# Kernel optimization log

Measured on AMD Instinct MI355X. Metric: run time of the kernel, lower is better.

The kernel has to match this reference:

```python
import jax, jax.numpy as jnp
import numpy as np

B, L, H = 512, 50, 128
HEADS, K = 8, 3
LP = 2.0            # l_p for LPPool1d
NUM_NODE = 250000


def setup_inputs() -> dict:
    key = jax.random.key(0)
    ks = jax.random.split(key, 24)
    s = 0.09  # ~1/sqrt(hidden) init as in reset_parameters
    p = lambda k, shp: jax.random.normal(k, shp, jnp.float32) * s
    return {
        "hidden": jax.random.normal(ks[0], (B, L, H), jnp.float32),
        "mask": jnp.ones((B, L), jnp.int32),
        "emb_w": p(ks[1], (NUM_NODE, H)),
        "pos_w": p(ks[2], (200, H)),
        "w1": p(ks[3], (2 * H, H)),
        "w2": p(ks[4], (H, 1)),
        "glu1_w": p(ks[5], (H, H)), "glu1_b": p(ks[6], (H,)),
        "glu2_w": p(ks[7], (H, H)),
        "lq_w0": p(ks[8], (H, H)), "lq_b0": p(ks[9], (H,)),
        "lq_w1": p(ks[10], (2 * H, H)), "lq_b1": p(ks[11], (H,)),
        "lq_w2": p(ks[12], (3 * H, H)), "lq_b2": p(ks[13], (H,)),
        "wz": p(ks[14], (H, H)), "bz": p(ks[15], (H,)),
        "wo": p(ks[16], (H, H)), "bo": p(ks[17], (H,)),
        "wt": p(ks[18], (H, H)), "bt": p(ks[19], (H,)),
        "lt2_w": p(ks[20], (2 * H, H)), "lt2_b": p(ks[21], (H,)),
    }


def reference(hidden, mask, emb_w, pos_w, w1, w2, glu1_w, glu1_b, glu2_w,
              lq_w0, lq_b0, lq_w1, lq_b1, lq_w2, lq_b2,
              wz, bz, wo, bo, wt, bt, lt2_w, lt2_b):
    Bc, Lc, Hc = hidden.shape
    dh = Hc // HEADS
    maskf = mask.astype(hidden.dtype)[:, :, None]          # [B,L,1]
    lengths = jnp.sum(mask, axis=1)                         # [B]

    # soft-attention readout (w_1 / w_2 / glu1 / glu2)
    pos = jnp.broadcast_to(pos_w[:Lc][None], (Bc, Lc, Hc))
    hs = jnp.sum(hidden * maskf, axis=1) / jnp.sum(maskf, axis=1)   # [B,H]
    nh = jnp.tanh(jnp.concatenate([pos, hidden], -1) @ w1)
    nh = jax.nn.sigmoid(nh @ glu1_w + glu1_b + (hs @ glu2_w)[:, None, :])
    beta = (nh @ w2) * maskf                                # [B,L,1]
    select = jnp.sum(beta * hidden, axis=1)                 # [B,H]

    # last-k item gathers feeding linear_q
    bidx = jnp.arange(Bc)
    def last_vec(j):
        idx = jnp.clip(lengths - (j + 1), -1, 1000)
        idx = jnp.where(idx < 0, idx + Lc, idx)  # torch negative-index wrap
        return hidden[bidx, idx]
    lasts = [last_vec(j) for j in range(K)]
    lq = [(lq_w0, lq_b0), (lq_w1, lq_b1), (lq_w2, lq_b2)]
    hts = jnp.stack([jnp.concatenate(lasts[:i + 1], -1) @ lq[i][0] + lq[i][1]
                     for i in range(K)], axis=1)            # [B,K,H]
    hts = hts / (jnp.linalg.norm(hts, axis=1, keepdims=True) + 1e-12)
    ht0 = hidden[bidx, lengths - 1]                         # [B,H]

    # LastAttenion (eval mode: dropout off); reshapes replicate torch .view
    q0 = (hts @ wz + bz).reshape(-1, K, dh)                 # [B*heads,K,dh]
    q1 = (hidden @ wo + bo).reshape(-1, Lc, dh)             # [B*heads,L,dh]
    q2 = (hidden @ wt + bt).reshape(-1, Lc, dh)
    alpha = jax.nn.sigmoid(jnp.einsum('bkd,bld->bkl', q0, q1))
    alpha = alpha.reshape(Bc, K * HEADS, Lc).transpose(0, 2, 1)  # [B,L,K*heads]
    alpha = jax.nn.softmax(2 * alpha, axis=1)
    # LPPool1d(norm=LP, kernel=K, stride=K) over last dim -> [B,L,heads]
    pooled = jnp.sum(alpha.reshape(Bc, Lc, HEADS, K) ** LP, axis=-1) ** (1.0 / LP)
    alpha = jnp.where(mask[:, :, None] > 0, pooled, -jnp.inf)
    alpha = jax.nn.softmax(2 * alpha, axis=1)               # [B,L,heads]
    q2r = q2.reshape(Bc, Lc, HEADS, dh)
    ais = jnp.sum((alpha[..., None] * q2r).reshape(Bc, Lc, Hc) * maskf, axis=1)  # [B,H]

    a = jnp.concatenate([ais, ht0], 1) @ lt2_w + lt2_b
    session = (select + a) * 0.5
    session = session / (jnp.linalg.norm(session, axis=1, keepdims=True) + 1e-12)
    b_items = emb_w[1:]
    b_items = b_items / (jnp.linalg.norm(b_items, axis=1, keepdims=True) + 1e-12)
    return 16.0 * (session @ b_items.T)                     # [B, num_node-1]
```

## Files before the change

### kernel.cpp

```cpp
#include <hip/hip_runtime.h>

#define LB 50
#define NITEMS 249999

__device__ __forceinline__ float sigm(float x){ return 1.0f/(1.0f + __expf(-x)); }

__device__ __forceinline__ unsigned int pack2(float x, float y){
  unsigned int a = __float_as_uint(x), b = __float_as_uint(y);
  a = (a + 0x7fffu + ((a>>16)&1u)) >> 16;
  b = (b + 0x7fffu + ((b>>16)&1u)) >> 16;
  return a | (b<<16);
}

__global__ void k_pos_part(const float* __restrict__ pos_w, const float* __restrict__ w1,
                           float* __restrict__ pos_part){
  int l = blockIdx.x, h = threadIdx.x;
  __shared__ float pr[128];
  pr[h] = pos_w[l*128 + h];
  __syncthreads();
  float s = 0.f;
  for (int j = 0; j < 128; ++j) s += pr[j] * w1[j*128 + h];
  pos_part[l*128 + h] = s;
}

__global__ void k_batch_prep(const float* __restrict__ hidden, const int* __restrict__ mask,
                             float* __restrict__ hs, float* __restrict__ lastsc,
                             float* __restrict__ ht0v){
  int b = blockIdx.x, h = threadIdx.x;
  const float* hb = hidden + (size_t)b*LB*128;
  const int* mb = mask + b*LB;
  int len = 0; float msum = 0.f, acc = 0.f;
  for (int l = 0; l < LB; ++l){
    int mi = mb[l];
    float mf = (float)mi;
    len += mi;
    msum += mf;
    acc += hb[l*128 + h] * mf;
  }
  hs[b*128+h] = acc / msum;
  for (int j = 0; j < 3; ++j){
    int idx = len - 1 - j;
    if (idx < -1) idx = -1;
    if (idx < 0) idx += LB;
    lastsc[b*384 + j*128 + h] = hb[idx*128 + h];
  }
  int i0 = len - 1; if (i0 < 0) i0 += LB;
  ht0v[b*128+h] = hb[i0*128 + h];
}

template<int MODE>
__global__ __launch_bounds__(256) void k_gemmA(const float* __restrict__ IN,
      const float* __restrict__ W, const float* __restrict__ extra,
      const float* __restrict__ w2, const int* __restrict__ mask,
      float* __restrict__ OUT){
  __shared__ float hidL[64*129];
  __shared__ float red[64*17];
  int t = threadIdx.x;
  int r0 = blockIdx.x * 64;
  for (int i = 0; i < 32; ++i){
    int p = i*256 + t;
    int row = p >> 7, k = p & 127;
    hidL[row*129 + k] = IN[(size_t)(r0+row)*128 + k];
  }
  __syncthreads();
  int tx = t & 15, ty = t >> 4;
  float acc[4][8];
#pragma unroll
  for (int m=0;m<4;++m)
#pragma unroll
    for (int c=0;c<8;++c) acc[m][c]=0.f;
  for (int k = 0; k < 128; ++k){
    float4 wa = *(const float4*)&W[k*128 + tx*4];
    float4 wb = *(const float4*)&W[k*128 + 64 + tx*4];
#pragma unroll
    for (int m = 0; m < 4; ++m){
      float a = hidL[(ty*4+m)*129 + k];
      acc[m][0] += a*wa.x; acc[m][1] += a*wa.y; acc[m][2] += a*wa.z; acc[m][3] += a*wa.w;
      acc[m][4] += a*wb.x; acc[m][5] += a*wb.y; acc[m][6] += a*wb.z; acc[m][7] += a*wb.w;
    }
  }
  if constexpr (MODE == 0){
#pragma unroll
    for (int m=0;m<4;++m){
      int r = r0 + ty*4 + m; int l = r % 50;
#pragma unroll
      for (int ci=0;ci<4;++ci){
        int c = tx*4+ci;
        OUT[(size_t)r*128 + c] = tanhf(acc[m][ci] + extra[l*128+c]);
        c = 64 + tx*4 + ci;
        OUT[(size_t)r*128 + c] = tanhf(acc[m][4+ci] + extra[l*128+c]);
      }
    }
  } else if constexpr (MODE == 1){
#pragma unroll
    for (int m=0;m<4;++m){
      int r = r0 + ty*4 + m; int bb = r / 50;
      float part = 0.f;
#pragma unroll
      for (int ci=0;ci<4;++ci){
        int c = tx*4+ci;
        float s = sigm(acc[m][ci] + extra[bb*128+c]); part += s * w2[c];
        c = 64 + tx*4 + ci;
        s = sigm(acc[m][4+ci] + extra[bb*128+c]); part += s * w2[c];
      }
      red[(ty*4+m)*17 + tx] = part;
    }
    __syncthreads();
    if (t < 64){
      float s = 0.f;
      for (int x=0;x<16;++x) s += red[t*17+x];
      int r = r0 + t;
      OUT[r] = s * (float)mask[r];
    }
  } else {
#pragma unroll
    for (int m=0;m<4;++m){
      int r = r0 + ty*4 + m;
#pragma unroll
      for (int ci=0;ci<4;++ci){
        int c = tx*4+ci;
        OUT[(size_t)r*128 + c] = acc[m][ci] + extra[c];
        c = 64 + tx*4 + ci;
        OUT[(size_t)r*128 + c] = acc[m][4+ci] + extra[c];
      }
    }
  }
}

__global__ void k_hsg(const float* __restrict__ hs, const float* __restrict__ glu2_w,
                      const float* __restrict__ glu1_b, float* __restrict__ hsg){
  int b = blockIdx.x, h = threadIdx.x;
  __shared__ float hl[128];
  hl[h] = hs[b*128+h];
  __syncthreads();
  float s = glu1_b[h];
  for (int j=0;j<128;++j) s += hl[j]*glu2_w[j*128+h];
  hsg[b*128+h] = s;
}

__global__ void k_select(const float* __restrict__ beta, const float* __restrict__ hidden,
                         float* __restrict__ sel){
  int b = blockIdx.x, h = threadIdx.x;
  float s = 0.f;
  for (int l=0;l<LB;++l) s += beta[b*LB+l]*hidden[((size_t)b*LB+l)*128 + h];
  sel[b*128+h] = s;
}

__global__ void k_hts_q0(const float* __restrict__ lastsc,
   const float* __restrict__ lq_w0, const float* __restrict__ lq_b0,
   const float* __restrict__ lq_w1, const float* __restrict__ lq_b1,
   const float* __restrict__ lq_w2, const float* __restrict__ lq_b2,
   const float* __restrict__ wz, const float* __restrict__ bz,
   float* __restrict__ q0f){
  int b = blockIdx.x, h = threadIdx.x;
  __shared__ float ll[384];
  __shared__ float htsL[384];
  for (int i=h;i<384;i+=128) ll[i]=lastsc[b*384+i];
  __syncthreads();
  float h0 = lq_b0[h], h1 = lq_b1[h], h2 = lq_b2[h];
  for (int j=0;j<128;++j) h0 += ll[j]*lq_w0[j*128+h];
  for (int j=0;j<256;++j) h1 += ll[j]*lq_w1[j*128+h];
  for (int j=0;j<384;++j) h2 += ll[j]*lq_w2[j*128+h];
  float nrm = sqrtf(h0*h0+h1*h1+h2*h2) + 1e-12f;
  htsL[h] = h0/nrm; htsL[128+h] = h1/nrm; htsL[256+h] = h2/nrm;
  __syncthreads();
  for (int k=0;k<3;++k){
    float s = bz[h];
    for (int j=0;j<128;++j) s += htsL[k*128+j]*wz[j*128+h];
    q0f[b*384 + k*128 + h] = s;
  }
}

__global__ __launch_bounds__(256) void k_attn(const float* __restrict__ q0f,
    const float* __restrict__ q1f, const float* __restrict__ q2f,
    const int* __restrict__ mask, float* __restrict__ ais){
  int b = blockIdx.x, t = threadIdx.x;
  __shared__ float q0L[384];
  __shared__ float q1L[6400];
  __shared__ float S[1200];
  __shared__ float A_[400];
  __shared__ float mkL[50];
  for (int i=t;i<384;i+=256) q0L[i]=q0f[b*384+i];
  for (int i=t;i<6400;i+=256) q1L[i]=q1f[(size_t)b*6400+i];
  if (t<50) mkL[t] = (float)mask[b*50+t];
  __syncthreads();
  for (int idx=t; idx<1200; idx+=256){
    int c = idx/50, l = idx - c*50;
    int g = c/3, kk = c - g*3;
    const float* q0p = q0L + 48*g + 16*kk;
    const float* q1p = q1L + 800*g + 16*l;
    float d = 0.f;
#pragma unroll
    for (int dd=0;dd<16;++dd) d += q0p[dd]*q1p[dd];
    S[c*50+l] = 2.f*sigm(d);
  }
  __syncthreads();
  if (t < 24){
    float m = -1e30f;
    for (int l=0;l<50;++l) m = fmaxf(m, S[t*50+l]);
    float s = 0.f;
    for (int l=0;l<50;++l){ float e=__expf(S[t*50+l]-m); S[t*50+l]=e; s+=e; }
    float inv = 1.f/s;
    for (int l=0;l<50;++l) S[t*50+l] *= inv;
  }
  __syncthreads();
  if (t < 8){
    int g = t;
    float m = -1e30f;
    for (int l=0;l<50;++l){
      float a0=S[(3*g+0)*50+l], a1=S[(3*g+1)*50+l], a2=S[(3*g+2)*50+l];
      float p = sqrtf(a0*a0+a1*a1+a2*a2);
      float v = (mkL[l] > 0.f) ? 2.f*p : -1e30f;
      A_[l*8+g]=v; m=fmaxf(m,v);
    }
    float s=0.f;
    for (int l=0;l<50;++l){ float e=__expf(A_[l*8+g]-m); A_[l*8+g]=e; s+=e; }
    float inv=1.f/s;
    for (int l=0;l<50;++l) A_[l*8+g]*=inv;
  }
  __syncthreads();
  if (t < 128){
    int h=t; float acc=0.f;
    for (int l=0;l<50;++l) acc += A_[l*8+(h>>4)] * q2f[((size_t)b*50+l)*128+h] * mkL[l];
    ais[b*128+h]=acc;
  }
}

__global__ void k_session(const float* __restrict__ ais, const float* __restrict__ ht0v,
   const float* __restrict__ sel, const float* __restrict__ lt2_w, const float* __restrict__ lt2_b,
   float* __restrict__ session){
  int b = blockIdx.x, h = threadIdx.x;
  __shared__ float aL[128];
  __shared__ float hL[128];
  __shared__ float red[128];
  aL[h]=ais[b*128+h]; hL[h]=ht0v[b*128+h];
  __syncthreads();
  float a = lt2_b[h];
  for (int j=0;j<128;++j) a += aL[j]*lt2_w[j*128+h];
  for (int j=0;j<128;++j) a += hL[j]*lt2_w[(128+j)*128+h];
  float s = (sel[b*128+h] + a)*0.5f;
  red[h]=s*s; __syncthreads();
  for (int off=64; off>0; off>>=1){
    if (h<off) red[h]+=red[h+off];
    __syncthreads();
  }
  session[b*128+h] = s / (sqrtf(red[0]) + 1e-12f);
}

__global__ __launch_bounds__(256) void k_invnorm(const float* __restrict__ emb, float* __restrict__ invn){
  int t = threadIdx.x;
  int row = blockIdx.x*4 + (t>>6);
  int lane = t & 63;
  if (row >= NITEMS) return;
  float2 v = *(const float2*)&emb[(size_t)(1+row)*128 + lane*2];
  float ss = v.x*v.x + v.y*v.y;
  for (int off=32; off; off>>=1) ss += __shfl_down(ss, off, 64);
  if (lane==0) invn[row] = 16.f/(sqrtf(ss)+1e-12f);
}

typedef short bhalf8 __attribute__((ext_vector_type(8)));
typedef float f32x4 __attribute__((ext_vector_type(4)));

__global__ __launch_bounds__(256) void k_out(const float* __restrict__ session,
    const float* __restrict__ emb, const float* __restrict__ invn, float* __restrict__ out){
  __shared__ unsigned int Ab[128*64];
  __shared__ unsigned int Bbuf[128*64];
  int t = threadIdx.x;
  int mb = blockIdx.x & 3, nb = blockIdx.x >> 2;
  int m0 = mb*128, n0 = nb*128;
  for (int i=0;i<32;++i){
    int p = i*256 + t;
    int row = p >> 6, kp = p & 63;
    float2 v = *(const float2*)&session[(size_t)(m0+row)*128 + kp*2];
    Ab[row*64 + (((kp>>2) ^ (row&7))<<2) + (kp&3)] = pack2(v.x, v.y);
  }
  for (int i=0;i<32;++i){
    int p = i*256 + t;
    int row = p >> 6, kp = p & 63;
    int item = n0 + row;
    float2 v = {0.f, 0.f};
    float sc = 0.f;
    if (item < NITEMS){ v = *(const float2*)&emb[(size_t)(1+item)*128 + kp*2]; sc = invn[item]; }
    Bbuf[row*64 + (((kp>>2) ^ (row&7))<<2) + (kp&3)] = pack2(v.x*sc, v.y*sc);
  }
  __syncthreads();
  int lane = t & 63, w = t >> 6;
  int r16 = lane & 15, quad = lane >> 4;
  f32x4 acc[2][8];
#pragma unroll
  for (int mi=0;mi<2;++mi)
#pragma unroll
    for (int ni=0;ni<8;++ni) acc[mi][ni] = (f32x4){0.f,0.f,0.f,0.f};
#pragma unroll
  for (int kc=0;kc<4;++kc){
    int gq = kc*4 + quad;
    bhalf8 af[2], bf[8];
#pragma unroll
    for (int mi=0;mi<2;++mi){
      int row = w*32 + mi*16 + r16;
      af[mi] = *(const bhalf8*)&Ab[row*64 + ((gq ^ (row&7))<<2)];
    }
#pragma unroll
    for (int ni=0;ni<8;++ni){
      int row = ni*16 + r16;
      bf[ni] = *(const bhalf8*)&Bbuf[row*64 + ((gq ^ (row&7))<<2)];
    }
#pragma unroll
    for (int mi=0;mi<2;++mi)
#pragma unroll
      for (int ni=0;ni<8;++ni)
        acc[mi][ni] = __builtin_amdgcn_mfma_f32_16x16x32_bf16(af[mi], bf[ni], acc[mi][ni], 0,0,0);
  }
#pragma unroll
  for (int mi=0;mi<2;++mi){
    int gr0 = m0 + w*32 + mi*16 + quad*4;
#pragma unroll
    for (int ni=0;ni<8;++ni){
      int gc = n0 + ni*16 + r16;
      if (gc < NITEMS){
#pragma unroll
        for (int r=0;r<4;++r) out[(size_t)(gr0+r)*NITEMS + gc] = acc[mi][ni][r];
      }
    }
  }
}

extern "C" void kernel_launch(void* const* d_in, const int* in_sizes, int n_in,
                              void* d_out, int out_size, void* d_ws, size_t ws_size,
                              hipStream_t stream){
  const float* hidden = (const float*)d_in[0];
  const int*   mask   = (const int*)d_in[1];
  const float* emb_w  = (const float*)d_in[2];
  const float* pos_w  = (const float*)d_in[3];
  const float* w1     = (const float*)d_in[4];
  const float* w2     = (const float*)d_in[5];
  const float* glu1_w = (const float*)d_in[6];
  const float* glu1_b = (const float*)d_in[7];
  const float* glu2_w = (const float*)d_in[8];
  const float* lq_w0  = (const float*)d_in[9];
  const float* lq_b0  = (const float*)d_in[10];
  const float* lq_w1  = (const float*)d_in[11];
  const float* lq_b1  = (const float*)d_in[12];
  const float* lq_w2  = (const float*)d_in[13];
  const float* lq_b2  = (const float*)d_in[14];
  const float* wz     = (const float*)d_in[15];
  const float* bz     = (const float*)d_in[16];
  const float* wo     = (const float*)d_in[17];
  const float* bo     = (const float*)d_in[18];
  const float* wt     = (const float*)d_in[19];
  const float* bt     = (const float*)d_in[20];
  const float* lt2_w  = (const float*)d_in[21];
  const float* lt2_b  = (const float*)d_in[22];
  float* outp = (float*)d_out;

  float* ws = (float*)d_ws;
  size_t o = 0;
  float* pos_part = ws + o; o += 50*128;
  float* hs       = ws + o; o += 512*128;
  float* hsg      = ws + o; o += 512*128;
  float* lastsc   = ws + o; o += 512*384;
  float* ht0v     = ws + o; o += 512*128;
  float* beta     = ws + o; o += 25600;
  float* sel      = ws + o; o += 512*128;
  float* q0f      = ws + o; o += 512*384;
  float* ais      = ws + o; o += 512*128;
  float* session  = ws + o; o += 512*128;
  float* invn     = ws + o; o += 250000;
  float* big1     = ws + o; o += (size_t)25600*128;
  float* big2     = ws + o; o += (size_t)25600*128;

  k_pos_part<<<50,128,0,stream>>>(pos_w, w1, pos_part);
  k_batch_prep<<<512,128,0,stream>>>(hidden, mask, hs, lastsc, ht0v);
  k_gemmA<0><<<400,256,0,stream>>>(hidden, w1 + 128*128, pos_part, nullptr, nullptr, big1);
  k_hsg<<<512,128,0,stream>>>(hs, glu2_w, glu1_b, hsg);
  k_gemmA<1><<<400,256,0,stream>>>(big1, glu1_w, hsg, w2, mask, beta);
  k_select<<<512,128,0,stream>>>(beta, hidden, sel);
  k_hts_q0<<<512,128,0,stream>>>(lastsc, lq_w0,lq_b0,lq_w1,lq_b1,lq_w2,lq_b2, wz, bz, q0f);
  k_gemmA<2><<<400,256,0,stream>>>(hidden, wo, bo, nullptr, nullptr, big1);
  k_gemmA<2><<<400,256,0,stream>>>(hidden, wt, bt, nullptr, nullptr, big2);
  k_attn<<<512,256,0,stream>>>(q0f, big1, big2, mask, ais);
  k_session<<<512,128,0,stream>>>(ais, ht0v, sel, lt2_w, lt2_b, session);
  k_invnorm<<<62500,256,0,stream>>>(emb_w, invn);
  k_out<<<7816,256,0,stream>>>(session, emb_w, invn, outp);
}
```

Measured before the change: 1.182 ms.

## Restructure output GEMM to keep item tile in registers and loop over batch

The final scoring GEMM now assigns each block 128 items for all 512 session rows. The normalized bf16 item fragments are held in registers and reused across four batch chunks, instead of reloading and re-converting the embedding tile for every batch chunk. The session vectors are pre-converted to bf16 in k_session and read directly from global/L2 without LDS staging. MFMA operands are swapped so each lane holds four consecutive output columns, which allows float4 output stores. This removes LDS traffic and quadruple embedding reads, at the cost of uncoalesced row-strided session loads and more register pressure.

```diff
diff --git a/kernel.cpp b/kernel.cpp
--- a/kernel.cpp
+++ b/kernel.cpp
@@ -10,6 +10,12 @@
   a = (a + 0x7fffu + ((a>>16)&1u)) >> 16;
   b = (b + 0x7fffu + ((b>>16)&1u)) >> 16;
   return a | (b<<16);
+}
+
+__device__ __forceinline__ unsigned short bf16of(float x){
+  unsigned int a = __float_as_uint(x);
+  a = (a + 0x7fffu + ((a>>16)&1u)) >> 16;
+  return (unsigned short)a;
 }
 
 __global__ void k_pos_part(const float* __restrict__ pos_w, const float* __restrict__ w1,
@@ -228,7 +234,7 @@
 
 __global__ void k_session(const float* __restrict__ ais, const float* __restrict__ ht0v,
    const float* __restrict__ sel, const float* __restrict__ lt2_w, const float* __restrict__ lt2_b,
-   float* __restrict__ session){
+   float* __restrict__ session, unsigned short* __restrict__ sbf){
   int b = blockIdx.x, h = threadIdx.x;
   __shared__ float aL[128];
   __shared__ float hL[128];
@@ -244,7 +250,9 @@
     if (h<off) red[h]+=red[h+off];
     __syncthreads();
   }
-  session[b*128+h] = s / (sqrtf(red[0]) + 1e-12f);
+  float v = s / (sqrtf(red[0]) + 1e-12f);
+  session[b*128+h] = v;
+  sbf[b*128+h] = bf16of(v);
 }
 
 __global__ __launch_bounds__(256) void k_invnorm(const float* __restrict__ emb, float* __restrict__ invn){
@@ -261,65 +269,73 @@
 typedef short bhalf8 __attribute__((ext_vector_type(8)));
 typedef float f32x4 __attribute__((ext_vector_type(4)));
 
-__global__ __launch_bounds__(256) void k_out(const float* __restrict__ session,
+struct f4a { float x, y, z, w; };
+
+__global__ __launch_bounds__(256) void k_out(const unsigned short* __restrict__ sbf,
     const float* __restrict__ emb, const float* __restrict__ invn, float* __restrict__ out){
-  __shared__ unsigned int Ab[128*64];
-  __shared__ unsigned int Bbuf[128*64];
   int t = threadIdx.x;
-  int mb = blockIdx.x & 3, nb = blockIdx.x >> 2;
-  int m0 = mb*128, n0 = nb*128;
-  for (int i=0;i<32;++i){
-    int p = i*256 + t;
-    int row = p >> 6, kp = p & 63;
-    float2 v = *(const float2*)&session[(size_t)(m0+row)*128 + kp*2];
-    Ab[row*64 + (((kp>>2) ^ (row&7))<<2) + (kp&3)] = pack2(v.x, v.y);
-  }
-  for (int i=0;i<32;++i){
-    int p = i*256 + t;
-    int row = p >> 6, kp = p & 63;
-    int item = n0 + row;
-    float2 v = {0.f, 0.f};
-    float sc = 0.f;
-    if (item < NITEMS){ v = *(const float2*)&emb[(size_t)(1+item)*128 + kp*2]; sc = invn[item]; }
-    Bbuf[row*64 + (((kp>>2) ^ (row&7))<<2) + (kp&3)] = pack2(v.x*sc, v.y*sc);
-  }
-  __syncthreads();
+  int n0 = blockIdx.x * 128;
   int lane = t & 63, w = t >> 6;
   int r16 = lane & 15, quad = lane >> 4;
-  f32x4 acc[2][8];
-#pragma unroll
-  for (int mi=0;mi<2;++mi)
-#pragma unroll
-    for (int ni=0;ni<8;++ni) acc[mi][ni] = (f32x4){0.f,0.f,0.f,0.f};
-#pragma unroll
-  for (int kc=0;kc<4;++kc){
-    int gq = kc*4 + quad;
-    bhalf8 af[2], bf[8];
-#pragma unroll
-    for (int mi=0;mi<2;++mi){
-      int row = w*32 + mi*16 + r16;
-      af[mi] = *(const bhalf8*)&Ab[row*64 + ((gq ^ (row&7))<<2)];
-    }
-#pragma unroll
-    for (int ni=0;ni<8;++ni){
-      int row = ni*16 + r16;
-      bf[ni] = *(const bhalf8*)&Bbuf[row*64 + ((gq ^ (row&7))<<2)];
-    }
-#pragma unroll
-    for (int mi=0;mi<2;++mi)
-#pragma unroll
-      for (int ni=0;ni<8;++ni)
-        acc[mi][ni] = __builtin_amdgcn_mfma_f32_16x16x32_bf16(af[mi], bf[ni], acc[mi][ni], 0,0,0);
-  }
-#pragma unroll
-  for (int mi=0;mi<2;++mi){
-    int gr0 = m0 + w*32 + mi*16 + quad*4;
-#pragma unroll
-    for (int ni=0;ni<8;++ni){
-      int gc = n0 + ni*16 + r16;
-      if (gc < NITEMS){
-#pragma unroll
-        for (int r=0;r<4;++r) out[(size_t)(gr0+r)*NITEMS + gc] = acc[mi][ni][r];
+
+  bhalf8 ef[2][4];
+#pragma unroll
+  for (int ni2=0; ni2<2; ++ni2){
+    int item = n0 + w*32 + ni2*16 + r16;
+    float s = (item < NITEMS) ? invn[item] : 0.f;
+    const float* ep = emb + (size_t)(1+item)*128 + quad*8;
+#pragma unroll
+    for (int kc=0; kc<4; ++kc){
+      float4 v0 = {0.f,0.f,0.f,0.f}, v1 = {0.f,0.f,0.f,0.f};
+      if (item < NITEMS){
+        v0 = *(const float4*)(ep + kc*32);
+        v1 = *(const float4*)(ep + kc*32 + 4);
+      }
+      union { bhalf8 h; unsigned int u[4]; } cv;
+      cv.u[0] = pack2(v0.x*s, v0.y*s);
+      cv.u[1] = pack2(v0.z*s, v0.w*s);
+      cv.u[2] = pack2(v1.x*s, v1.y*s);
+      cv.u[3] = pack2(v1.z*s, v1.w*s);
+      ef[ni2][kc] = cv.h;
+    }
+  }
+
+#pragma unroll
+  for (int mb=0; mb<4; ++mb){
+    f32x4 acc[2][8];
+#pragma unroll
+    for (int ni2=0; ni2<2; ++ni2)
+#pragma unroll
+      for (int mi=0; mi<8; ++mi) acc[ni2][mi] = (f32x4){0.f,0.f,0.f,0.f};
+
+#pragma unroll
+    for (int kc=0; kc<4; ++kc){
+      bhalf8 bf[8];
+#pragma unroll
+      for (int mi=0; mi<8; ++mi)
+        bf[mi] = *(const bhalf8*)&sbf[(size_t)(mb*128 + mi*16 + r16)*128 + kc*32 + quad*8];
+#pragma unroll
+      for (int mi=0; mi<8; ++mi){
+        acc[0][mi] = __builtin_amdgcn_mfma_f32_16x16x32_bf16(ef[0][kc], bf[mi], acc[0][mi], 0,0,0);
+        acc[1][mi] = __builtin_amdgcn_mfma_f32_16x16x32_bf16(ef[1][kc], bf[mi], acc[1][mi], 0,0,0);
+      }
+    }
+
+#pragma unroll
+    for (int ni2=0; ni2<2; ++ni2){
+      int n = n0 + w*32 + ni2*16 + quad*4;
+#pragma unroll
+      for (int mi=0; mi<8; ++mi){
+        int m = mb*128 + mi*16 + r16;
+        size_t off = (size_t)m*NITEMS + n;
+        if (n + 3 < NITEMS){
+          f4a v; v.x = acc[ni2][mi][0]; v.y = acc[ni2][mi][1];
+                 v.z = acc[ni2][mi][2]; v.w = acc[ni2][mi][3];
+          *(f4a*)&out[off] = v;
+        } else {
+#pragma unroll
+          for (int r=0; r<4; ++r) if (n + r < NITEMS) out[off+r] = acc[ni2][mi][r];
+        }
       }
     }
   }
@@ -365,6 +381,7 @@
   float* q0f      = ws + o; o += 512*384;
   float* ais      = ws + o; o += 512*128;
   float* session  = ws + o; o += 512*128;
+  unsigned short* sbf = (unsigned short*)(ws + o); o += 512*128/2;
   float* invn     = ws + o; o += 250000;
   float* big1     = ws + o; o += (size_t)25600*128;
   float* big2     = ws + o; o += (size_t)25600*128;
@@ -379,7 +396,7 @@
   k_gemmA<2><<<400,256,0,stream>>>(hidden, wo, bo, nullptr, nullptr, big1);
   k_gemmA<2><<<400,256,0,stream>>>(hidden, wt, bt, nullptr, nullptr, big2);
   k_attn<<<512,256,0,stream>>>(q0f, big1, big2, mask, ais);
-  k_session<<<512,128,0,stream>>>(ais, ht0v, sel, lt2_w, lt2_b, session);
+  k_session<<<512,128,0,stream>>>(ais, ht0v, sel, lt2_w, lt2_b, session, sbf);
   k_invnorm<<<62500,256,0,stream>>>(emb_w, invn);
-  k_out<<<7816,256,0,stream>>>(session, emb_w, invn, outp);
-}
+  k_out<<<1954,256,0,stream>>>(sbf, emb_w, invn, outp);
+}
```

Result: faster. 981.7 us (-17.0%).
